# Performance work log

Measured on AMD Instinct MI355X. Metric: run time of the kernel, lower is better.

## Reference

```python
import jax, jax.numpy as jnp
import numpy as np

E, T, D, I, G, K = 8, 1024, 1024, 5632, 128, 2  # experts, tokens, hidden, intermediate, gptq group, topk
RENORMALIZE = True


def setup_inputs() -> dict:
    key = jax.random.key(0)
    ks = jax.random.split(key, 6)
    x = jax.random.normal(ks[0], (T, D), dtype=jnp.float32)
    gating_output = jax.random.normal(ks[1], (T, E), dtype=jnp.float32)
    # int4 GPTQ nibbles stored as int32 in [0, 16)
    w1_q = jax.random.randint(ks[2], (E, D, 2 * I), 0, 16, dtype=jnp.int32)
    w2_q = jax.random.randint(ks[3], (E, I, D), 0, 16, dtype=jnp.int32)
    # per-group scales (group size G along the input/contraction dim)
    w1_scale = jax.random.uniform(ks[4], (E, D // G, 2 * I), dtype=jnp.float32) * 0.02
    w2_scale = jax.random.uniform(ks[5], (E, I // G, D), dtype=jnp.float32) * 0.02
    return {"x": x, "gating_output": gating_output, "w1_q": w1_q, "w2_q": w2_q,
            "w1_scale": w1_scale, "w2_scale": w2_scale}


def _dequant(q, scale, group_size):
    # symmetric GPTQ int4: w = (q - 8) * scale, scale broadcast over its group
    s = jnp.repeat(scale, group_size, axis=1)  # [E, Kdim, N]
    return (q.astype(scale.dtype) - 8.0) * s


def reference(x, gating_output, w1_q, w2_q, w1_scale, w2_scale):
    w1 = _dequant(w1_q, w1_scale, G)  # [E, D, 2I]
    w2 = _dequant(w2_q, w2_scale, G)  # [E, I, D]

    # top-k softmax routing (use_grouped_topk=False path)
    probs = jax.nn.softmax(gating_output, axis=-1)        # [T, E]
    topk_w, topk_i = jax.lax.top_k(probs, K)              # [T, K]
    if RENORMALIZE:
        topk_w = topk_w / jnp.sum(topk_w, axis=-1, keepdims=True)
    # dense combine weights [T, E] (zero where expert not selected)
    cw = jnp.sum(jax.nn.one_hot(topk_i, E, dtype=x.dtype) * topk_w[..., None], axis=1)

    # expert MLPs: silu(x @ Wg) * (x @ Wu) @ Wd
    h = jnp.einsum('td,edn->etn', x, w1)                  # [E, T, 2I]
    gate, up = h[..., :I], h[..., I:]
    act = jax.nn.silu(gate) * up                          # [E, T, I]
    y = jnp.einsum('eti,eid->etd', act, w2)               # [E, T, D]

    out = jnp.einsum('te,etd->td', cw, y)                 # [T, D]
    return out
```

## Files before the change

### kernel.cpp

```cpp
#include <hip/hip_runtime.h>
#include <cstdint>
#include <cstddef>

#define E_ 8
#define T_ 1024
#define D_ 1024
#define I_ 5632
#define TWO_I_ 11264
#define NPAD_MAX 2176
#define NGRP_MAX 136

#define WS_ACTF_B 65536
#define WS_XGF_B  (65536 + 24510464)
#define WS_Y_B    WS_XGF_B
#define WS_CNT   0
#define WS_BASEP 8
#define WS_ESLOT 16
#define WS_TOKW  2064
#define WS_ETOK  4112

typedef __attribute__((ext_vector_type(8))) __bf16 bf16x8;
typedef __attribute__((ext_vector_type(4))) float  f32x4;

__device__ __forceinline__ unsigned f2bf(float f) {
    unsigned u = __float_as_uint(f);
    u += 0x7fffu + ((u >> 16) & 1u);
    return u >> 16;
}
__device__ __forceinline__ unsigned pack2bf(float f0, float f1) {
    unsigned a0 = __float_as_uint(f0); a0 += 0x7fffu + ((a0 >> 16) & 1u);
    unsigned a1 = __float_as_uint(f1); a1 += 0x7fffu + ((a1 >> 16) & 1u);
    return (a0 >> 16) | (a1 & 0xffff0000u);
}
#define QC(P, c) ((c) == 0 ? (P).x : (c) == 1 ? (P).y : (c) == 2 ? (P).z : (P).w)

__global__ void routing_kernel(const float* __restrict__ gate,
                               int* cnt, int* basep, int* eslot,
                               float* tokw, int* etok)
{
    int t = threadIdx.x;
    if (t < E_) cnt[t] = 0;
    __syncthreads();
    float g[E_];
#pragma unroll
    for (int e = 0; e < E_; ++e) g[e] = gate[t * E_ + e];
    int i0 = 0; float p0 = g[0];
#pragma unroll
    for (int e = 1; e < E_; ++e) if (g[e] > p0) { p0 = g[e]; i0 = e; }
    int i1 = -1; float p1 = -1e30f;
#pragma unroll
    for (int e = 0; e < E_; ++e) if (e != i0 && g[e] > p1) { p1 = g[e]; i1 = e; }
    float w0 = 1.0f / (1.0f + expf(p1 - p0));
    float w1 = 1.0f - w0;
    int s0 = atomicAdd(&cnt[i0], 1);
    int s1 = atomicAdd(&cnt[i1], 1);
    etok[i0 * T_ + s0] = t;
    etok[i1 * T_ + s1] = t;
    eslot[t * 2 + 0] = i0 * T_ + s0;  tokw[t * 2 + 0] = w0;
    eslot[t * 2 + 1] = i1 * T_ + s1;  tokw[t * 2 + 1] = w1;
    __syncthreads();
    if (t == 0) {
        int r = 0;
#pragma unroll
        for (int e = 0; e < E_; ++e) { basep[e] = r; r += (cnt[e] + 15) & ~15; }
    }
}

__global__ void gather_cast_kernel(const float* __restrict__ x,
                                   const int* __restrict__ cnt,
                                   const int* __restrict__ basep,
                                   const int* __restrict__ etok,
                                   unsigned short* __restrict__ xgf)
{
    int e = blockIdx.x >> 6, g = blockIdx.x & 63;
    int n = cnt[e];
    if (g * 16 >= n) return;
    int tid = threadIdx.x;
    int row = g * 16 + (tid & 15);
    row = min(row, n - 1);
    int tok = etok[e * T_ + row];
    const float* xr = x + (size_t)tok * D_;
    unsigned short* dst = xgf + ((size_t)(basep[e] >> 4) + g) * 16384;
#pragma unroll
    for (int it = 0; it < 8; ++it) {
        int c = it * 16 + (tid >> 4);
        float4 v0 = *(const float4*)(xr + c * 8);
        float4 v1 = *(const float4*)(xr + c * 8 + 4);
        uint4 h;
        h.x = pack2bf(v0.x, v0.y); h.y = pack2bf(v0.z, v0.w);
        h.z = pack2bf(v1.x, v1.y); h.w = pack2bf(v1.z, v1.w);
        *(uint4*)(dst + c * 128 + (tid & 15) * 8) = h;
    }
}

__global__ __launch_bounds__(512, 2) void gemm1_kernel(
    const unsigned short* __restrict__ xgf, const int* __restrict__ w1q,
    const float* __restrict__ w1s, const int* __restrict__ cnt,
    const int* __restrict__ basep, unsigned short* __restrict__ actf)
{
    __shared__ unsigned char blds[2][32768];
    int cg = blockIdx.x % 44, e = blockIdx.x / 44;
    int n = cnt[e];
    if (n <= 0) return;
    int npad = (n + 15) & ~15;
    int pb = basep[e];
    int tid = threadIdx.x, lane = tid & 63, w = tid >> 6;
    int l15 = lane & 15, lq = lane >> 4;
    int colg = w & 3, mh = w >> 2;

    int colq = lane, kc = w;
    int col0 = colq * 4;
    int jb = (col0 < 128) ? (cg * 128 + col0) : (I_ + cg * 128 + (col0 - 128));
    const int*   gq  = w1q + (size_t)e * 1024 * TWO_I_ + jb;
    const float* sqp = w1s + (size_t)e * 8 * TWO_I_ + jb;
    int fcw  = colq >> 2;
    int pzw  = (fcw & 3) | ((fcw >> 2) << 4);
    int lanp = (kc & 3) * 16 + (colq & 3) * 4;
    unsigned wro[4];
#pragma unroll
    for (int c = 0; c < 4; ++c)
        wro[c] = (unsigned)(fcw * 2048 + (kc >> 2) * 1024 + (((lanp + c) ^ pzw) << 4));

    unsigned rdo[4];
#pragma unroll
    for (int nf = 0; nf < 4; ++nf) {
        int fc = (nf < 2) ? (2 * colg + nf) : (8 + 2 * colg + (nf - 2));
        int pz = (fc & 3) | ((fc >> 2) << 4);
        rdo[nf] = (unsigned)(fc * 2048 + ((lane ^ pz) << 4));
    }

    int4  Pa[8], Pb[8];
    float4 Sa, Sb;

#define G1_ISSUE(S, P, SS)                                                  \
    { const int* gp_ = gq + (size_t)((S) * 64 + kc * 8) * TWO_I_;           \
      _Pragma("unroll")                                                     \
      for (int j_ = 0; j_ < 8; ++j_)                                        \
          P[j_] = *(const int4*)(gp_ + (size_t)j_ * TWO_I_);                \
      SS = *(const float4*)(sqp + (size_t)((S) >> 1) * TWO_I_); }

#define G1_DEQW(S, P, SS)                                                   \
    { unsigned char* bp_ = &blds[(S) & 1][0];                               \
      _Pragma("unroll")                                                     \
      for (int c_ = 0; c_ < 4; ++c_) {                                      \
          float s_ = QC(SS, c_);                                            \
          float o_ = -8.f * s_;                                             \
          uint4 h_;                                                         \
          h_.x = pack2bf((float)QC(P[0], c_) * s_ + o_, (float)QC(P[1], c_) * s_ + o_); \
          h_.y = pack2bf((float)QC(P[2], c_) * s_ + o_, (float)QC(P[3], c_) * s_ + o_); \
          h_.z = pack2bf((float)QC(P[4], c_) * s_ + o_, (float)QC(P[5], c_) * s_ + o_); \
          h_.w = pack2bf((float)QC(P[6], c_) * s_ + o_, (float)QC(P[7], c_) * s_ + o_); \
          *(uint4*)(bp_ + wro[c_]) = h_;                                    \
      } }

#define G1_STAGE(S, PD, SD, PI, SI)                                         \
    { const char* at_ = abase + (size_t)(S) * 2048;                         \
      bf16x8 a0_[4], a1_[4];                                                \
      _Pragma("unroll")                                                     \
      for (int mi_ = 0; mi_ < 4; ++mi_) a0_[mi_] = *(const bf16x8*)(at_ + aoff[mi_]); \
      _Pragma("unroll")                                                     \
      for (int mi_ = 0; mi_ < 4; ++mi_) a1_[mi_] = *(const bf16x8*)(at_ + 1024 + aoff[mi_]); \
      __builtin_amdgcn_sched_barrier(0);                                    \
      if ((S) + 2 < 16) { G1_ISSUE((S) + 2, PI, SI) }                       \
      __builtin_amdgcn_sched_barrier(0);                                    \
      const unsigned char* bp_ = &blds[(S) & 1][0];                         \
      __builtin_amdgcn_s_setprio(1);                                        \
      _Pragma("unroll")                                                     \
      for (int nf_ = 0; nf_ < 4; ++nf_) {                                   \
          bf16x8 b0_ = *(const bf16x8*)(bp_ + rdo[nf_]);                    \
          bf16x8 b1_ = *(const bf16x8*)(bp_ + rdo[nf_] + 1024);             \
          _Pragma("unroll")                                                 \
          for (int mi_ = 0; mi_ < 4; ++mi_) {                               \
              acc[mi_][nf_] = __builtin_amdgcn_mfma_f32_16x16x32_bf16(a0_[mi_], b0_, acc[mi_][nf_], 0, 0, 0); \
              acc[mi_][nf_] = __builtin_amdgcn_mfma_f32_16x16x32_bf16(a1_[mi_], b1_, acc[mi_][nf_], 0, 0, 0); \
          } }                                                               \
      __builtin_amdgcn_s_setprio(0);                                        \
      if ((S) + 1 < 16) { G1_DEQW((S) + 1, PD, SD) }                        \
      asm volatile("s_waitcnt lgkmcnt(0)" ::: "memory");                    \
      __builtin_amdgcn_s_barrier();                                         \
      asm volatile("" ::: "memory"); }

    const char* abase = (const char*)xgf + lq * 256 + l15 * 16;

    for (int tb = 0; tb < npad; tb += 128) {
        int aoff[4];
#pragma unroll
        for (int mi = 0; mi < 4; ++mi) {
            int R = tb + mh * 64 + mi * 16;
            R = min(R, npad - 16);
            aoff[mi] = ((pb + R) >> 4) * 32768;
        }
        f32x4 acc[4][4];
#pragma unroll
        for (int mi = 0; mi < 4; ++mi)
#pragma unroll
            for (int nf = 0; nf < 4; ++nf)
                acc[mi][nf] = (f32x4){0.f, 0.f, 0.f, 0.f};

        G1_ISSUE(0, Pa, Sa)
        G1_ISSUE(1, Pb, Sb)
        G1_DEQW(0, Pa, Sa)
        asm volatile("s_waitcnt lgkmcnt(0)" ::: "memory");
        __builtin_amdgcn_s_barrier();
        asm volatile("" ::: "memory");

#pragma unroll 1
        for (int s2 = 0; s2 < 8; ++s2) {
            G1_STAGE(2 * s2,     Pb, Sb, Pa, Sa)
            G1_STAGE(2 * s2 + 1, Pa, Sa, Pb, Sb)
        }

#pragma unroll
        for (int mi = 0; mi < 4; ++mi) {
#pragma unroll
            for (int r = 0; r < 4; ++r) {
                int m = tb + mh * 64 + mi * 16 + lq * 4 + r;
                if (m < npad) {
                    int prow = pb + m;
                    size_t rg = (size_t)(prow >> 4) * 90112 + (prow & 15) * 8;
#pragma unroll
                    for (int nf = 0; nf < 2; ++nf) {
                        float gv = acc[mi][nf][r], uv = acc[mi][nf + 2][r];
                        float av = gv / (1.f + __expf(-gv)) * uv;
                        int icol = cg * 128 + (2 * colg + nf) * 16 + l15;
                        actf[rg + (icol >> 3) * 128 + (icol & 7)] = (unsigned short)f2bf(av);
                    }
                }
            }
        }
    }
#undef G1_ISSUE
#undef G1_DEQW
#undef G1_STAGE
}

__global__ __launch_bounds__(512, 2) void gemm2_kernel(
    const unsigned short* __restrict__ actf, const int* __restrict__ w2q,
    const float* __restrict__ w2s, const int* __restrict__ cnt,
    const int* __restrict__ basep, float* __restrict__ y)
{
    __shared__ unsigned char blds[2][32768];
    int bid = blockIdx.x;
    int seg = bid & 3, dt = (bid >> 2) & 7, e = bid >> 5;
    int n = cnt[e];
    if (n <= 0) return;
    int npad = (n + 15) & ~15;
    int pb = basep[e];
    int tid = threadIdx.x, lane = tid & 63, w = tid >> 6;
    int l15 = lane & 15, lq = lane >> 4;
    int colg = w & 3, mh = w >> 2;

    int colq = tid & 31, kc = tid >> 5;
    const int*   gq  = w2q + ((size_t)e * 5632 + seg * 1408) * 1024 + dt * 128 + colq * 4;
    const float* sqp = w2s + ((size_t)e * 44 + seg * 11) * 1024 + dt * 128 + colq * 4;
    int fcw  = colq >> 2;
    int pzw  = (fcw & 3) | ((fcw >> 2) << 5);
    int lanp = (kc & 3) * 16 + (colq & 3) * 4;
    unsigned wro[4];
#pragma unroll
    for (int c = 0; c < 4; ++c)
        wro[c] = (unsigned)(fcw * 4096 + (kc >> 2) * 1024 + (((lanp + c) ^ pzw) << 4));

    unsigned rdo[2];
#pragma unroll
    for (int nf = 0; nf < 2; ++nf) {
        int fc = 2 * colg + nf;
        int pz = (fc & 3) | ((fc >> 2) << 5);
        rdo[nf] = (unsigned)(fc * 4096 + ((lane ^ pz) << 4));
    }

    int4  Pa[8], Pb[8];
    float4 Sa, Sb;

#define G2_ISSUE(S, P, SS)                                                  \
    { const int* gp_ = gq + (size_t)((S) * 128 + kc * 8) * 1024;            \
      _Pragma("unroll")                                                     \
      for (int j_ = 0; j_ < 8; ++j_)                                        \
          P[j_] = *(const int4*)(gp_ + (size_t)j_ * 1024);                  \
      SS = *(const float4*)(sqp + (size_t)(S) * 1024); }

#define G2_DEQW(S, P, SS)                                                   \
    { unsigned char* bp_ = &blds[(S) & 1][0];                               \
      _Pragma("unroll")                                                     \
      for (int c_ = 0; c_ < 4; ++c_) {                                      \
          float s_ = QC(SS, c_);                                            \
          float o_ = -8.f * s_;                                             \
          uint4 h_;                                                         \
          h_.x = pack2bf((float)QC(P[0], c_) * s_ + o_, (float)QC(P[1], c_) * s_ + o_); \
          h_.y = pack2bf((float)QC(P[2], c_) * s_ + o_, (float)QC(P[3], c_) * s_ + o_); \
          h_.z = pack2bf((float)QC(P[4], c_) * s_ + o_, (float)QC(P[5], c_) * s_ + o_); \
          h_.w = pack2bf((float)QC(P[6], c_) * s_ + o_, (float)QC(P[7], c_) * s_ + o_); \
          *(uint4*)(bp_ + wro[c_]) = h_;                                    \
      } }

#define G2_STAGE(S, PD, SD, PI, SI)                                         \
    { const char* at_ = abase + (size_t)(S) * 4096;                         \
      bf16x8 a_[4][4];                                                      \
      _Pragma("unroll")                                                     \
      for (int ss_ = 0; ss_ < 4; ++ss_)                                     \
          _Pragma("unroll")                                                 \
          for (int mi_ = 0; mi_ < 4; ++mi_)                                 \
              a_[ss_][mi_] = *(const bf16x8*)(at_ + ss_ * 1024 + aoff[mi_]); \
      __builtin_amdgcn_sched_barrier(0);                                    \
      if ((S) + 2 < 11) { G2_ISSUE((S) + 2, PI, SI) }                       \
      __builtin_amdgcn_sched_barrier(0);                                    \
      const unsigned char* bp_ = &blds[(S) & 1][0];                         \
      __builtin_amdgcn_s_setprio(1);                                        \
      _Pragma("unroll")                                                     \
      for (int nf_ = 0; nf_ < 2; ++nf_) {                                   \
          _Pragma("unroll")                                                 \
          for (int ss_ = 0; ss_ < 4; ++ss_) {                               \
              bf16x8 b_ = *(const bf16x8*)(bp_ + rdo[nf_] + ss_ * 1024);    \
              _Pragma("unroll")                                             \
              for (int mi_ = 0; mi_ < 4; ++mi_)                             \
                  acc[mi_][nf_] = __builtin_amdgcn_mfma_f32_16x16x32_bf16(a_[ss_][mi_], b_, acc[mi_][nf_], 0, 0, 0); \
          } }                                                               \
      __builtin_amdgcn_s_setprio(0);                                        \
      if ((S) + 1 < 11) { G2_DEQW((S) + 1, PD, SD) }                        \
      asm volatile("s_waitcnt lgkmcnt(0)" ::: "memory");                    \
      __builtin_amdgcn_s_barrier();                                         \
      asm volatile("" ::: "memory"); }

    const char* abase = (const char*)actf + seg * 45056 + lq * 256 + l15 * 16;

    for (int tb = 0; tb < npad; tb += 128) {
        int aoff[4];
#pragma unroll
        for (int mi = 0; mi < 4; ++mi) {
            int R = tb + mh * 64 + mi * 16;
            R = min(R, npad - 16);
            aoff[mi] = ((pb + R) >> 4) * 180224;
        }
        f32x4 acc[4][2];
#pragma unroll
        for (int mi = 0; mi < 4; ++mi)
#pragma unroll
            for (int nf = 0; nf < 2; ++nf)
                acc[mi][nf] = (f32x4){0.f, 0.f, 0.f, 0.f};

        G2_ISSUE(0, Pa, Sa)
        G2_ISSUE(1, Pb, Sb)
        G2_DEQW(0, Pa, Sa)
        asm volatile("s_waitcnt lgkmcnt(0)" ::: "memory");
        __builtin_amdgcn_s_barrier();
        asm volatile("" ::: "memory");

#pragma unroll 1
        for (int s2 = 0; s2 < 5; ++s2) {
            G2_STAGE(2 * s2,     Pb, Sb, Pa, Sa)
            G2_STAGE(2 * s2 + 1, Pa, Sa, Pb, Sb)
        }
        G2_STAGE(10, Pb, Sb, Pa, Sa)

#pragma unroll
        for (int mi = 0; mi < 4; ++mi) {
#pragma unroll
            for (int r = 0; r < 4; ++r) {
                int m = tb + mh * 64 + mi * 16 + lq * 4 + r;
                if (m < n) {
                    float* yr = y + ((size_t)seg * NPAD_MAX + pb + m) * 1024;
                    int dc = dt * 128 + colg * 32 + l15;
                    yr[dc]      = acc[mi][0][r];
                    yr[dc + 16] = acc[mi][1][r];
                }
            }
        }
    }
#undef G2_ISSUE
#undef G2_DEQW
#undef G2_STAGE
}

__global__ void combine_kernel(const float* __restrict__ y,
                               const int* __restrict__ eslot,
                               const float* __restrict__ tokw,
                               const int* __restrict__ basep,
                               float* __restrict__ out)
{
    int idx = blockIdx.x * blockDim.x + threadIdx.x;
    int t  = idx >> 8;
    int dc = idx & 255;
    int es0 = eslot[t * 2 + 0], es1 = eslot[t * 2 + 1];
    float w0 = tokw[t * 2 + 0], w1 = tokw[t * 2 + 1];
    int p0 = basep[es0 >> 10] + (es0 & 1023);
    int p1 = basep[es1 >> 10] + (es1 & 1023);
    const float4* y4 = (const float4*)y;
    float4 o = (float4){0.f, 0.f, 0.f, 0.f};
#pragma unroll
    for (int seg = 0; seg < 4; ++seg) {
        float4 a = y4[((size_t)seg * NPAD_MAX + p0) * 256 + dc];
        float4 b = y4[((size_t)seg * NPAD_MAX + p1) * 256 + dc];
        o.x += w0 * a.x + w1 * b.x;
        o.y += w0 * a.y + w1 * b.y;
        o.z += w0 * a.z + w1 * b.z;
        o.w += w0 * a.w + w1 * b.w;
    }
    ((float4*)out)[idx] = o;
}

extern "C" void kernel_launch(void* const* d_in, const int* in_sizes, int n_in,
                              void* d_out, int out_size, void* d_ws, size_t ws_size,
                              hipStream_t stream)
{
    const float* x    = (const float*)d_in[0];
    const float* gate = (const float*)d_in[1];
    const int*   w1q  = (const int*)d_in[2];
    const int*   w2q  = (const int*)d_in[3];
    const float* w1s  = (const float*)d_in[4];
    const float* w2s  = (const float*)d_in[5];
    float* out = (float*)d_out;
    int*   wsi = (int*)d_ws;
    float* wsf = (float*)d_ws;

    int*   cnt   = wsi + WS_CNT;
    int*   basep = wsi + WS_BASEP;
    int*   eslot = wsi + WS_ESLOT;
    float* tokw  = wsf + WS_TOKW;
    int*   etok  = wsi + WS_ETOK;
    unsigned short* actf = (unsigned short*)((char*)d_ws + WS_ACTF_B);
    unsigned short* xgf  = (unsigned short*)((char*)d_ws + WS_XGF_B);
    float*          y    = (float*)((char*)d_ws + WS_Y_B);

    routing_kernel<<<1, 1024, 0, stream>>>(gate, cnt, basep, eslot, tokw, etok);
    gather_cast_kernel<<<E_ * 64, 256, 0, stream>>>(x, cnt, basep, etok, xgf);
    gemm1_kernel<<<E_ * 44, 512, 0, stream>>>(xgf, w1q, w1s, cnt, basep, actf);
    gemm2_kernel<<<E_ * 8 * 4, 512, 0, stream>>>(actf, w2q, w2s, cnt, basep, y);
    combine_kernel<<<(T_ * D_ / 4) / 256, 256, 0, stream>>>(y, eslot, tokw, basep, out);
}
```

Before: 866.4 us.

## Split MoE GEMMs into smaller 256-thread blocks with row-block parallelism and XCD-aware mapping

Both dequant-GEMM kernels drop from 512-thread blocks with 128-row tiles to 256-thread blocks with 64-row tiles and halved column or K-step widths. The grid is widened by a factor of 5 along the token-row dimension and remapped so that blocks sharing an expert/column tile land on the same XCD. The goal is more concurrent blocks, better CU occupancy, and better L2 locality for the int4 weight stream. In exchange, each weight tile is dequantized and loaded by more blocks, and the two-deep register prefetch becomes single-buffered.

```diff
diff --git a/kernel.cpp b/kernel.cpp
--- a/kernel.cpp
+++ b/kernel.cpp
@@ -93,58 +93,60 @@
     }
 }
 
-__global__ __launch_bounds__(512, 2) void gemm1_kernel(
+__global__ __launch_bounds__(256, 3) void gemm1_kernel(
     const unsigned short* __restrict__ xgf, const int* __restrict__ w1q,
     const float* __restrict__ w1s, const int* __restrict__ cnt,
     const int* __restrict__ basep, unsigned short* __restrict__ actf)
 {
-    __shared__ unsigned char blds[2][32768];
-    int cg = blockIdx.x % 44, e = blockIdx.x / 44;
+    __shared__ unsigned char blds[2][16384];
+    int b = blockIdx.x;
+    int xcd = b & 7, sl = b >> 3;
+    int q5 = sl / 5, rb = sl - q5 * 5;
+    int cb = q5 * 8 + xcd;
+    int e = cb / 88, cg = cb - e * 88;
+
     int n = cnt[e];
     if (n <= 0) return;
     int npad = (n + 15) & ~15;
+    if (rb * 64 >= npad) return;
     int pb = basep[e];
+
     int tid = threadIdx.x, lane = tid & 63, w = tid >> 6;
     int l15 = lane & 15, lq = lane >> 4;
-    int colg = w & 3, mh = w >> 2;
-
-    int colq = lane, kc = w;
-    int col0 = colq * 4;
-    int jb = (col0 < 128) ? (cg * 128 + col0) : (I_ + cg * 128 + (col0 - 128));
-    const int*   gq  = w1q + (size_t)e * 1024 * TWO_I_ + jb;
+
+    int colq = tid & 31, kc = tid >> 5;
+    int bcol = colq * 4;
+    int jb = (bcol < 64) ? (cg * 64 + bcol) : (I_ + cg * 64 + (bcol - 64));
+    const int*   gq  = w1q + ((size_t)e * 1024 + kc * 8) * TWO_I_ + jb;
     const float* sqp = w1s + (size_t)e * 8 * TWO_I_ + jb;
     int fcw  = colq >> 2;
     int pzw  = (fcw & 3) | ((fcw >> 2) << 4);
     int lanp = (kc & 3) * 16 + (colq & 3) * 4;
+    unsigned wbase = (unsigned)fcw * 2048 + (unsigned)(kc >> 2) * 1024;
     unsigned wro[4];
 #pragma unroll
     for (int c = 0; c < 4; ++c)
-        wro[c] = (unsigned)(fcw * 2048 + (kc >> 2) * 1024 + (((lanp + c) ^ pzw) << 4));
-
-    unsigned rdo[4];
-#pragma unroll
-    for (int nf = 0; nf < 4; ++nf) {
-        int fc = (nf < 2) ? (2 * colg + nf) : (8 + 2 * colg + (nf - 2));
-        int pz = (fc & 3) | ((fc >> 2) << 4);
-        rdo[nf] = (unsigned)(fc * 2048 + ((lane ^ pz) << 4));
-    }
-
-    int4  Pa[8], Pb[8];
-    float4 Sa, Sb;
-
-#define G1_ISSUE(S, P, SS)                                                  \
-    { const int* gp_ = gq + (size_t)((S) * 64 + kc * 8) * TWO_I_;           \
-      _Pragma("unroll")                                                     \
+        wro[c] = wbase + (unsigned)(((lanp + c) ^ pzw) << 4);
+
+    unsigned rg0 = (unsigned)w * 2048 + (unsigned)((lane ^ w) << 4);
+    int pzu = w | 16;
+    unsigned ru0 = (unsigned)(w + 4) * 2048 + (unsigned)((lane ^ pzu) << 4);
+
+    const char* abase = (const char*)xgf + lane * 16;
+
+    int4 P[8]; float4 SS;
+
+#define G1_ISSUE(S)                                                         \
+    { _Pragma("unroll")                                                     \
       for (int j_ = 0; j_ < 8; ++j_)                                        \
-          P[j_] = *(const int4*)(gp_ + (size_t)j_ * TWO_I_);                \
+          P[j_] = *(const int4*)(gq + (size_t)((S) * 64 + j_) * TWO_I_);    \
       SS = *(const float4*)(sqp + (size_t)((S) >> 1) * TWO_I_); }
 
-#define G1_DEQW(S, P, SS)                                                   \
+#define G1_DEQW(S)                                                          \
     { unsigned char* bp_ = &blds[(S) & 1][0];                               \
       _Pragma("unroll")                                                     \
       for (int c_ = 0; c_ < 4; ++c_) {                                      \
-          float s_ = QC(SS, c_);                                            \
-          float o_ = -8.f * s_;                                             \
+          float s_ = QC(SS, c_); float o_ = -8.f * s_;                      \
           uint4 h_;                                                         \
           h_.x = pack2bf((float)QC(P[0], c_) * s_ + o_, (float)QC(P[1], c_) * s_ + o_); \
           h_.y = pack2bf((float)QC(P[2], c_) * s_ + o_, (float)QC(P[3], c_) * s_ + o_); \
@@ -153,138 +155,136 @@
           *(uint4*)(bp_ + wro[c_]) = h_;                                    \
       } }
 
-#define G1_STAGE(S, PD, SD, PI, SI)                                         \
-    { const char* at_ = abase + (size_t)(S) * 2048;                         \
-      bf16x8 a0_[4], a1_[4];                                                \
-      _Pragma("unroll")                                                     \
-      for (int mi_ = 0; mi_ < 4; ++mi_) a0_[mi_] = *(const bf16x8*)(at_ + aoff[mi_]); \
-      _Pragma("unroll")                                                     \
-      for (int mi_ = 0; mi_ < 4; ++mi_) a1_[mi_] = *(const bf16x8*)(at_ + 1024 + aoff[mi_]); \
-      __builtin_amdgcn_sched_barrier(0);                                    \
-      if ((S) + 2 < 16) { G1_ISSUE((S) + 2, PI, SI) }                       \
-      __builtin_amdgcn_sched_barrier(0);                                    \
-      const unsigned char* bp_ = &blds[(S) & 1][0];                         \
-      __builtin_amdgcn_s_setprio(1);                                        \
-      _Pragma("unroll")                                                     \
-      for (int nf_ = 0; nf_ < 4; ++nf_) {                                   \
-          bf16x8 b0_ = *(const bf16x8*)(bp_ + rdo[nf_]);                    \
-          bf16x8 b1_ = *(const bf16x8*)(bp_ + rdo[nf_] + 1024);             \
-          _Pragma("unroll")                                                 \
-          for (int mi_ = 0; mi_ < 4; ++mi_) {                               \
-              acc[mi_][nf_] = __builtin_amdgcn_mfma_f32_16x16x32_bf16(a0_[mi_], b0_, acc[mi_][nf_], 0, 0, 0); \
-              acc[mi_][nf_] = __builtin_amdgcn_mfma_f32_16x16x32_bf16(a1_[mi_], b1_, acc[mi_][nf_], 0, 0, 0); \
-          } }                                                               \
-      __builtin_amdgcn_s_setprio(0);                                        \
-      if ((S) + 1 < 16) { G1_DEQW((S) + 1, PD, SD) }                        \
-      asm volatile("s_waitcnt lgkmcnt(0)" ::: "memory");                    \
-      __builtin_amdgcn_s_barrier();                                         \
-      asm volatile("" ::: "memory"); }
-
-    const char* abase = (const char*)xgf + lq * 256 + l15 * 16;
-
-    for (int tb = 0; tb < npad; tb += 128) {
+    for (int tb = rb * 64; tb < npad; tb += 320) {
         int aoff[4];
 #pragma unroll
         for (int mi = 0; mi < 4; ++mi) {
-            int R = tb + mh * 64 + mi * 16;
+            int R = tb + mi * 16;
             R = min(R, npad - 16);
             aoff[mi] = ((pb + R) >> 4) * 32768;
         }
-        f32x4 acc[4][4];
-#pragma unroll
-        for (int mi = 0; mi < 4; ++mi)
-#pragma unroll
-            for (int nf = 0; nf < 4; ++nf)
-                acc[mi][nf] = (f32x4){0.f, 0.f, 0.f, 0.f};
-
-        G1_ISSUE(0, Pa, Sa)
-        G1_ISSUE(1, Pb, Sb)
-        G1_DEQW(0, Pa, Sa)
+        f32x4 accg[4], accu[4];
+#pragma unroll
+        for (int mi = 0; mi < 4; ++mi) {
+            accg[mi] = (f32x4){0.f, 0.f, 0.f, 0.f};
+            accu[mi] = (f32x4){0.f, 0.f, 0.f, 0.f};
+        }
+
+        G1_ISSUE(0)
+        G1_DEQW(0)
         asm volatile("s_waitcnt lgkmcnt(0)" ::: "memory");
         __builtin_amdgcn_s_barrier();
         asm volatile("" ::: "memory");
 
-#pragma unroll 1
-        for (int s2 = 0; s2 < 8; ++s2) {
-            G1_STAGE(2 * s2,     Pb, Sb, Pa, Sa)
-            G1_STAGE(2 * s2 + 1, Pa, Sa, Pb, Sb)
+#pragma unroll 2
+        for (int st = 0; st < 16; ++st) {
+            const char* at = abase + (size_t)st * 2048;
+            bf16x8 a0[4], a1[4];
+#pragma unroll
+            for (int mi = 0; mi < 4; ++mi)
+                a0[mi] = *(const bf16x8*)(at + aoff[mi]);
+#pragma unroll
+            for (int mi = 0; mi < 4; ++mi)
+                a1[mi] = *(const bf16x8*)(at + 1024 + aoff[mi]);
+            if (st + 1 < 16) { G1_ISSUE(st + 1) }
+            const unsigned char* bp = &blds[st & 1][0];
+            bf16x8 bg0 = *(const bf16x8*)(bp + rg0);
+            bf16x8 bu0 = *(const bf16x8*)(bp + ru0);
+            bf16x8 bg1 = *(const bf16x8*)(bp + rg0 + 1024);
+            bf16x8 bu1 = *(const bf16x8*)(bp + ru0 + 1024);
+            __builtin_amdgcn_s_setprio(1);
+#pragma unroll
+            for (int mi = 0; mi < 4; ++mi) {
+                accg[mi] = __builtin_amdgcn_mfma_f32_16x16x32_bf16(a0[mi], bg0, accg[mi], 0, 0, 0);
+                accu[mi] = __builtin_amdgcn_mfma_f32_16x16x32_bf16(a0[mi], bu0, accu[mi], 0, 0, 0);
+            }
+#pragma unroll
+            for (int mi = 0; mi < 4; ++mi) {
+                accg[mi] = __builtin_amdgcn_mfma_f32_16x16x32_bf16(a1[mi], bg1, accg[mi], 0, 0, 0);
+                accu[mi] = __builtin_amdgcn_mfma_f32_16x16x32_bf16(a1[mi], bu1, accu[mi], 0, 0, 0);
+            }
+            __builtin_amdgcn_s_setprio(0);
+            if (st + 1 < 16) { G1_DEQW(st + 1) }
+            asm volatile("s_waitcnt lgkmcnt(0)" ::: "memory");
+            __builtin_amdgcn_s_barrier();
+            asm volatile("" ::: "memory");
         }
 
 #pragma unroll
         for (int mi = 0; mi < 4; ++mi) {
 #pragma unroll
             for (int r = 0; r < 4; ++r) {
-                int m = tb + mh * 64 + mi * 16 + lq * 4 + r;
+                int m = tb + mi * 16 + lq * 4 + r;
                 if (m < npad) {
+                    float gv = accg[mi][r], uv = accu[mi][r];
+                    float av = gv / (1.f + __expf(-gv)) * uv;
                     int prow = pb + m;
-                    size_t rg = (size_t)(prow >> 4) * 90112 + (prow & 15) * 8;
-#pragma unroll
-                    for (int nf = 0; nf < 2; ++nf) {
-                        float gv = acc[mi][nf][r], uv = acc[mi][nf + 2][r];
-                        float av = gv / (1.f + __expf(-gv)) * uv;
-                        int icol = cg * 128 + (2 * colg + nf) * 16 + l15;
-                        actf[rg + (icol >> 3) * 128 + (icol & 7)] = (unsigned short)f2bf(av);
-                    }
+                    int icol = cg * 64 + w * 16 + l15;
+                    size_t o = (size_t)(prow >> 4) * 90112 + (icol >> 3) * 128
+                             + (prow & 15) * 8 + (icol & 7);
+                    actf[o] = (unsigned short)f2bf(av);
                 }
             }
         }
     }
 #undef G1_ISSUE
 #undef G1_DEQW
-#undef G1_STAGE
-}
-
-__global__ __launch_bounds__(512, 2) void gemm2_kernel(
+}
+
+__global__ __launch_bounds__(256, 3) void gemm2_kernel(
     const unsigned short* __restrict__ actf, const int* __restrict__ w2q,
     const float* __restrict__ w2s, const int* __restrict__ cnt,
     const int* __restrict__ basep, float* __restrict__ y)
 {
-    __shared__ unsigned char blds[2][32768];
-    int bid = blockIdx.x;
-    int seg = bid & 3, dt = (bid >> 2) & 7, e = bid >> 5;
+    __shared__ unsigned char blds[2][16384];
+    int b = blockIdx.x;
+    int xcd = b & 7, sl = b >> 3;
+    int q5 = sl / 5, rb = sl - q5 * 5;
+    int cb = q5 * 8 + xcd;
+    int e = cb >> 5, r5 = cb & 31;
+    int dt = r5 >> 2, seg = r5 & 3;
+
     int n = cnt[e];
     if (n <= 0) return;
     int npad = (n + 15) & ~15;
+    if (rb * 64 >= npad) return;
     int pb = basep[e];
+
     int tid = threadIdx.x, lane = tid & 63, w = tid >> 6;
     int l15 = lane & 15, lq = lane >> 4;
-    int colg = w & 3, mh = w >> 2;
 
     int colq = tid & 31, kc = tid >> 5;
-    const int*   gq  = w2q + ((size_t)e * 5632 + seg * 1408) * 1024 + dt * 128 + colq * 4;
-    const float* sqp = w2s + ((size_t)e * 44 + seg * 11) * 1024 + dt * 128 + colq * 4;
+    int colb = dt * 128 + colq * 4;
+    const int*   gq  = w2q + ((size_t)e * 5632 + seg * 1408 + kc * 8) * 1024 + colb;
+    const float* sqp = w2s + ((size_t)e * 44 + seg * 11) * 1024 + colb;
     int fcw  = colq >> 2;
-    int pzw  = (fcw & 3) | ((fcw >> 2) << 5);
+    int pzw  = (fcw & 3) | ((fcw >> 2) << 4);
     int lanp = (kc & 3) * 16 + (colq & 3) * 4;
+    unsigned wbase = (unsigned)fcw * 2048 + (unsigned)(kc >> 2) * 1024;
     unsigned wro[4];
 #pragma unroll
     for (int c = 0; c < 4; ++c)
-        wro[c] = (unsigned)(fcw * 4096 + (kc >> 2) * 1024 + (((lanp + c) ^ pzw) << 4));
-
-    unsigned rdo[2];
-#pragma unroll
-    for (int nf = 0; nf < 2; ++nf) {
-        int fc = 2 * colg + nf;
-        int pz = (fc & 3) | ((fc >> 2) << 5);
-        rdo[nf] = (unsigned)(fc * 4096 + ((lane ^ pz) << 4));
-    }
-
-    int4  Pa[8], Pb[8];
-    float4 Sa, Sb;
-
-#define G2_ISSUE(S, P, SS)                                                  \
-    { const int* gp_ = gq + (size_t)((S) * 128 + kc * 8) * 1024;            \
-      _Pragma("unroll")                                                     \
+        wro[c] = wbase + (unsigned)(((lanp + c) ^ pzw) << 4);
+
+    unsigned rg0 = (unsigned)w * 2048 + (unsigned)((lane ^ w) << 4);
+    int pzu = w | 16;
+    unsigned ru0 = (unsigned)(w + 4) * 2048 + (unsigned)((lane ^ pzu) << 4);
+
+    const char* abase = (const char*)actf + seg * 45056 + lane * 16;
+
+    int4 P[8]; float4 SS;
+
+#define G2_ISSUE(S)                                                         \
+    { _Pragma("unroll")                                                     \
       for (int j_ = 0; j_ < 8; ++j_)                                        \
-          P[j_] = *(const int4*)(gp_ + (size_t)j_ * 1024);                  \
-      SS = *(const float4*)(sqp + (size_t)(S) * 1024); }
-
-#define G2_DEQW(S, P, SS)                                                   \
+          P[j_] = *(const int4*)(gq + (size_t)((S) * 64 + j_) * 1024);      \
+      SS = *(const float4*)(sqp + (size_t)((S) >> 1) * 1024); }
+
+#define G2_DEQW(S)                                                          \
     { unsigned char* bp_ = &blds[(S) & 1][0];                               \
       _Pragma("unroll")                                                     \
       for (int c_ = 0; c_ < 4; ++c_) {                                      \
-          float s_ = QC(SS, c_);                                            \
-          float o_ = -8.f * s_;                                             \
+          float s_ = QC(SS, c_); float o_ = -8.f * s_;                      \
           uint4 h_;                                                         \
           h_.x = pack2bf((float)QC(P[0], c_) * s_ + o_, (float)QC(P[1], c_) * s_ + o_); \
           h_.y = pack2bf((float)QC(P[2], c_) * s_ + o_, (float)QC(P[3], c_) * s_ + o_); \
@@ -293,82 +293,77 @@
           *(uint4*)(bp_ + wro[c_]) = h_;                                    \
       } }
 
-#define G2_STAGE(S, PD, SD, PI, SI)                                         \
-    { const char* at_ = abase + (size_t)(S) * 4096;                         \
-      bf16x8 a_[4][4];                                                      \
-      _Pragma("unroll")                                                     \
-      for (int ss_ = 0; ss_ < 4; ++ss_)                                     \
-          _Pragma("unroll")                                                 \
-          for (int mi_ = 0; mi_ < 4; ++mi_)                                 \
-              a_[ss_][mi_] = *(const bf16x8*)(at_ + ss_ * 1024 + aoff[mi_]); \
-      __builtin_amdgcn_sched_barrier(0);                                    \
-      if ((S) + 2 < 11) { G2_ISSUE((S) + 2, PI, SI) }                       \
-      __builtin_amdgcn_sched_barrier(0);                                    \
-      const unsigned char* bp_ = &blds[(S) & 1][0];                         \
-      __builtin_amdgcn_s_setprio(1);                                        \
-      _Pragma("unroll")                                                     \
-      for (int nf_ = 0; nf_ < 2; ++nf_) {                                   \
-          _Pragma("unroll")                                                 \
-          for (int ss_ = 0; ss_ < 4; ++ss_) {                               \
-              bf16x8 b_ = *(const bf16x8*)(bp_ + rdo[nf_] + ss_ * 1024);    \
-              _Pragma("unroll")                                             \
-              for (int mi_ = 0; mi_ < 4; ++mi_)                             \
-                  acc[mi_][nf_] = __builtin_amdgcn_mfma_f32_16x16x32_bf16(a_[ss_][mi_], b_, acc[mi_][nf_], 0, 0, 0); \
-          } }                                                               \
-      __builtin_amdgcn_s_setprio(0);                                        \
-      if ((S) + 1 < 11) { G2_DEQW((S) + 1, PD, SD) }                        \
-      asm volatile("s_waitcnt lgkmcnt(0)" ::: "memory");                    \
-      __builtin_amdgcn_s_barrier();                                         \
-      asm volatile("" ::: "memory"); }
-
-    const char* abase = (const char*)actf + seg * 45056 + lq * 256 + l15 * 16;
-
-    for (int tb = 0; tb < npad; tb += 128) {
+    for (int tb = rb * 64; tb < npad; tb += 320) {
         int aoff[4];
 #pragma unroll
         for (int mi = 0; mi < 4; ++mi) {
-            int R = tb + mh * 64 + mi * 16;
+            int R = tb + mi * 16;
             R = min(R, npad - 16);
             aoff[mi] = ((pb + R) >> 4) * 180224;
         }
-        f32x4 acc[4][2];
-#pragma unroll
-        for (int mi = 0; mi < 4; ++mi)
-#pragma unroll
-            for (int nf = 0; nf < 2; ++nf)
-                acc[mi][nf] = (f32x4){0.f, 0.f, 0.f, 0.f};
-
-        G2_ISSUE(0, Pa, Sa)
-        G2_ISSUE(1, Pb, Sb)
-        G2_DEQW(0, Pa, Sa)
+        f32x4 acc0[4], acc1[4];
+#pragma unroll
+        for (int mi = 0; mi < 4; ++mi) {
+            acc0[mi] = (f32x4){0.f, 0.f, 0.f, 0.f};
+            acc1[mi] = (f32x4){0.f, 0.f, 0.f, 0.f};
+        }
+
+        G2_ISSUE(0)
+        G2_DEQW(0)
         asm volatile("s_waitcnt lgkmcnt(0)" ::: "memory");
         __builtin_amdgcn_s_barrier();
         asm volatile("" ::: "memory");
 
-#pragma unroll 1
-        for (int s2 = 0; s2 < 5; ++s2) {
-            G2_STAGE(2 * s2,     Pb, Sb, Pa, Sa)
-            G2_STAGE(2 * s2 + 1, Pa, Sa, Pb, Sb)
-        }
-        G2_STAGE(10, Pb, Sb, Pa, Sa)
+#pragma unroll 2
+        for (int st = 0; st < 22; ++st) {
+            const char* at = abase + (size_t)st * 2048;
+            bf16x8 a0[4], a1[4];
+#pragma unroll
+            for (int mi = 0; mi < 4; ++mi)
+                a0[mi] = *(const bf16x8*)(at + aoff[mi]);
+#pragma unroll
+            for (int mi = 0; mi < 4; ++mi)
+                a1[mi] = *(const bf16x8*)(at + 1024 + aoff[mi]);
+            if (st + 1 < 22) { G2_ISSUE(st + 1) }
+            const unsigned char* bp = &blds[st & 1][0];
+            bf16x8 b00 = *(const bf16x8*)(bp + rg0);
+            bf16x8 b10 = *(const bf16x8*)(bp + ru0);
+            bf16x8 b01 = *(const bf16x8*)(bp + rg0 + 1024);
+            bf16x8 b11 = *(const bf16x8*)(bp + ru0 + 1024);
+            __builtin_amdgcn_s_setprio(1);
+#pragma unroll
+            for (int mi = 0; mi < 4; ++mi) {
+                acc0[mi] = __builtin_amdgcn_mfma_f32_16x16x32_bf16(a0[mi], b00, acc0[mi], 0, 0, 0);
+                acc1[mi] = __builtin_amdgcn_mfma_f32_16x16x32_bf16(a0[mi], b10, acc1[mi], 0, 0, 0);
+            }
+#pragma unroll
+            for (int mi = 0; mi < 4; ++mi) {
+                acc0[mi] = __builtin_amdgcn_mfma_f32_16x16x32_bf16(a1[mi], b01, acc0[mi], 0, 0, 0);
+                acc1[mi] = __builtin_amdgcn_mfma_f32_16x16x32_bf16(a1[mi], b11, acc1[mi], 0, 0, 0);
+            }
+            __builtin_amdgcn_s_setprio(0);
+            if (st + 1 < 22) { G2_DEQW(st + 1) }
+            asm volatile("s_waitcnt lgkmcnt(0)" ::: "memory");
+            __builtin_amdgcn_s_barrier();
+            asm volatile("" ::: "memory");
+        }
 
 #pragma unroll
         for (int mi = 0; mi < 4; ++mi) {
 #pragma unroll
             for (int r = 0; r < 4; ++r) {
-                int m = tb + mh * 64 + mi * 16 + lq * 4 + r;
+                int m = tb + mi * 16 + lq * 4 + r;
                 if (m < n) {
                     float* yr = y + ((size_t)seg * NPAD_MAX + pb + m) * 1024;
-                    int dc = dt * 128 + colg * 32 + l15;
-                    yr[dc]      = acc[mi][0][r];
-                    yr[dc + 16] = acc[mi][1][r];
+                    int dc = dt * 128 + w * 16 + l15;
+                    yr[dc]      = acc0[mi][r];
+                    yr[dc + 64] = acc1[mi][r];
                 }
             }
         }
     }
 #undef G2_ISSUE
 #undef G2_DEQW
-#undef G2_STAGE
 }
 
 __global__ void combine_kernel(const float* __restrict__ y,
@@ -423,7 +418,7 @@
 
     routing_kernel<<<1, 1024, 0, stream>>>(gate, cnt, basep, eslot, tokw, etok);
     gather_cast_kernel<<<E_ * 64, 256, 0, stream>>>(x, cnt, basep, etok, xgf);
-    gemm1_kernel<<<E_ * 44, 512, 0, stream>>>(xgf, w1q, w1s, cnt, basep, actf);
-    gemm2_kernel<<<E_ * 8 * 4, 512, 0, stream>>>(actf, w2q, w2s, cnt, basep, y);
+    gemm1_kernel<<<E_ * 88 * 5, 256, 0, stream>>>(xgf, w1q, w1s, cnt, basep, actf);
+    gemm2_kernel<<<E_ * 8 * 4 * 5, 256, 0, stream>>>(actf, w2q, w2s, cnt, basep, y);
     combine_kernel<<<(T_ * D_ / 4) / 256, 256, 0, stream>>>(y, eslot, tokw, basep, out);
 }
```

Result: faster. 817.6 us (-5.6%).
